# Kernel optimization log

Measured on AMD Instinct MI355X. Metric: run time of the kernel, lower is better.

Reference implementation:

```python
import jax, jax.numpy as jnp
import numpy as np

B, S, H = 1, 2048, 1024
NH, HD = 16, 64          # num heads, head dim (H = NH*HD)
NT = 1024                # param token num (qkv_slot_num = proj_slot_num)


def pattention(x, key_tokens, value_tokens):
    """Pattention with gelu_l2_norm: x:[...,H] -> [...,out]."""
    attn = jnp.einsum('bsh,th->bst', x, key_tokens)          # scale_factor = 1
    g = jax.nn.gelu(attn, approximate=False)                 # torch F.gelu exact
    norm = jnp.linalg.norm(g, axis=-1, keepdims=True)
    w = g / norm * jnp.sqrt(jnp.asarray(g.shape[-1], g.dtype))
    return jnp.einsum('bst,td->bsd', w, value_tokens)


def setup_inputs() -> dict:
    key = jax.random.key(0)
    ks = jax.random.split(key, 9)
    names = ['q_key', 'q_val', 'k_key', 'k_val', 'v_key', 'v_val', 'proj_key', 'proj_val']
    inp = {'x': jax.random.normal(ks[0], (B, S, H), jnp.float32)}
    for i, n in enumerate(names):
        inp[n] = jax.random.normal(ks[i + 1], (NT, H), jnp.float32) * 0.02
    return inp


def reference(x, q_key, q_val, k_key, k_val, v_key, v_val, proj_key, proj_val):
    # Q/K/V via Pattention (token-parameter attention)
    q = pattention(x, q_key, q_val).reshape(B, S, NH, HD)
    k = pattention(x, k_key, k_val).reshape(B, S, NH, HD)
    v = pattention(x, v_key, v_val).reshape(B, S, NH, HD)
    # causal softmax attention, scale = 1/sqrt(head_dim) (flash default)
    scale = 1.0 / jnp.sqrt(jnp.asarray(HD, q.dtype))
    scores = jnp.einsum('bqhd,bkhd->bhqk', q, k) * scale
    causal = jnp.tril(jnp.ones((S, S), dtype=bool))
    scores = jnp.where(causal, scores, jnp.asarray(-1e30, scores.dtype))
    probs = jax.nn.softmax(scores, axis=-1)
    ctx = jnp.einsum('bhqk,bkhd->bqhd', probs, v).reshape(B, S, H)
    # output projection via Pattention
    return pattention(ctx, proj_key, proj_val)
```

## Files before the change

### kernel.cpp

```cpp
#include <hip/hip_runtime.h>
#include <cstdint>
#include <cstddef>

#define S_LEN 2048
#define H_DIM 1024
#define NTOK  1024
#define NHEAD 16
#define HDIM  64

typedef __bf16 bf16;
typedef __bf16 bf16x8 __attribute__((ext_vector_type(8)));
typedef __bf16 bf16x4 __attribute__((ext_vector_type(4)));
typedef float  f32x4  __attribute__((ext_vector_type(4)));

static __device__ __forceinline__ f32x4 mfma16(bf16x8 a, bf16x8 b, f32x4 c) {
    return __builtin_amdgcn_mfma_f32_16x16x32_bf16(a, b, c, 0, 0, 0);
}

static __device__ __forceinline__ void async16(const void* gp, void* lp) {
    __builtin_amdgcn_global_load_lds(
        (const __attribute__((address_space(1))) void*)gp,
        (__attribute__((address_space(3))) void*)lp, 16, 0, 0);
}

struct ConvArgs {
    const float* src[6];
    bf16* dst[6];
};
__global__ __launch_bounds__(256) void convert6(ConvArgs a) {
    const float* __restrict__ s = a.src[blockIdx.y];
    bf16* __restrict__ d = a.dst[blockIdx.y];
    size_t i = ((size_t)blockIdx.x * 256 + threadIdx.x) * 4;
    f32x4 v = *(const f32x4*)&s[i];
    bf16x4 o;
    o[0] = (bf16)v[0]; o[1] = (bf16)v[1]; o[2] = (bf16)v[2]; o[3] = (bf16)v[3];
    *(bf16x4*)&d[i] = o;
}

struct TcArgs {
    const float* src[4];
    bf16* dst[4];
};
__global__ void transpose_cvt(TcArgs a) {
    const float* __restrict__ in = a.src[blockIdx.z];
    bf16* __restrict__ out = a.dst[blockIdx.z];
    __shared__ float t[32][33];
    const int bx = blockIdx.x * 32, by = blockIdx.y * 32;
    const int x = threadIdx.x, y = threadIdx.y;
#pragma unroll
    for (int j = 0; j < 32; j += 8)
        t[y + j][x] = in[(size_t)(by + y + j) * 1024 + bx + x];
    __syncthreads();
#pragma unroll
    for (int j = 0; j < 32; j += 8)
        out[(size_t)(bx + y + j) * 1024 + by + x] = (bf16)t[x][y + j];
}

template <int MODE, typename OutT>
struct GemmArgs {
    const bf16* A[3];
    const bf16* B[3];
    OutT* C[3];
};

template <int MODE, typename OutT>
__global__ __launch_bounds__(256, 3) void gemm_bt(GemmArgs<MODE, OutT> args) {
    constexpr int Kd = 1024, Nd = 1024, BK = 64;
    const bf16* __restrict__ A = args.A[blockIdx.z];
    const bf16* __restrict__ B = args.B[blockIdx.z];
    OutT* __restrict__ C = args.C[blockIdx.z];

    __shared__ __align__(16) bf16 As[2][128 * BK];
    __shared__ __align__(16) bf16 Bs[2][64 * BK];

    const int tid = threadIdx.x;
    const int w = tid >> 6, lane = tid & 63, quad = lane >> 4, m16 = lane & 15;
    const int wm = (w >> 1) * 64, wn = (w & 1) * 32;
    const int bm = blockIdx.y * 128, bn = blockIdx.x * 64;

    const int srow = lane >> 3;
    const int sseg = ((lane & 7) ^ srow) * 8;

    auto stage = [&](int buf, int k0) {
        const bf16* Ab = A + (size_t)bm * Kd + k0;
#pragma unroll
        for (int c = 0; c < 4; ++c) {
            int chunk = w * 4 + c;
            async16(Ab + (size_t)(chunk * 8 + srow) * Kd + sseg,
                    &As[buf][chunk * 512]);
        }
        const bf16* Bb = B + (size_t)bn * Kd + k0;
#pragma unroll
        for (int c = 0; c < 2; ++c) {
            int chunk = w * 2 + c;
            async16(Bb + (size_t)(chunk * 8 + srow) * Kd + sseg,
                    &Bs[buf][chunk * 512]);
        }
    };

    f32x4 acc[4][2] = {};
    stage(0, 0);

    for (int k0 = 0; k0 < Kd; k0 += BK) {
        const int buf = (k0 >> 6) & 1;
        asm volatile("s_waitcnt vmcnt(0)" ::: "memory");
        __syncthreads();
        if (k0 + BK < Kd) stage(buf ^ 1, k0 + BK);

        bf16x8 a[2][4], b[2][2];
#pragma unroll
        for (int kc = 0; kc < 2; ++kc) {
#pragma unroll
            for (int i = 0; i < 4; ++i) {
                int row = wm + i * 16 + m16;
                a[kc][i] = *(const bf16x8*)
                    &As[buf][row * 64 + (((kc * 4 + quad) ^ (row & 7)) << 3)];
            }
#pragma unroll
            for (int j = 0; j < 2; ++j) {
                int row = wn + j * 16 + m16;
                b[kc][j] = *(const bf16x8*)
                    &Bs[buf][row * 64 + (((kc * 4 + quad) ^ (row & 7)) << 3)];
            }
        }
#pragma unroll
        for (int kc = 0; kc < 2; ++kc)
#pragma unroll
            for (int i = 0; i < 4; ++i)
#pragma unroll
                for (int j = 0; j < 2; ++j)
                    acc[i][j] = mfma16(a[kc][i], b[kc][j], acc[i][j]);
    }

#pragma unroll
    for (int i = 0; i < 4; ++i)
#pragma unroll
        for (int j = 0; j < 2; ++j)
#pragma unroll
            for (int r = 0; r < 4; ++r) {
                int row = bm + wm + i * 16 + quad * 4 + r;
                int col = bn + wn + j * 16 + m16;
                float v = acc[i][j][r];
                if (MODE == 1)
                    v = 0.5f * v * (1.0f + erff(v * 0.70710678118654752f));
                C[(size_t)row * Nd + col] = (OutT)v;
            }
}

struct NormArgs { bf16* G[3]; };
__global__ __launch_bounds__(256) void rownorm_kernel(NormArgs na) {
    __shared__ float wsum[4];
    bf16* __restrict__ G = na.G[blockIdx.y];
    const int s = blockIdx.x, tid = threadIdx.x;
    bf16* row = G + (size_t)s * 1024;
    bf16x4 g = *(const bf16x4*)&row[tid * 4];
    float f0 = (float)g[0], f1 = (float)g[1], f2 = (float)g[2], f3 = (float)g[3];
    float ss = f0 * f0 + f1 * f1 + f2 * f2 + f3 * f3;
#pragma unroll
    for (int sh = 1; sh < 64; sh <<= 1) ss += __shfl_xor(ss, sh);
    if ((tid & 63) == 0) wsum[tid >> 6] = ss;
    __syncthreads();
    float total = wsum[0] + wsum[1] + wsum[2] + wsum[3];
    float scale = 32.0f * rsqrtf(total);
    bf16x4 o;
    o[0] = (bf16)(f0 * scale); o[1] = (bf16)(f1 * scale);
    o[2] = (bf16)(f2 * scale); o[3] = (bf16)(f3 * scale);
    *(bf16x4*)&row[tid * 4] = o;
}

__global__ __launch_bounds__(256, 3) void flash_kernel(
    const bf16* __restrict__ Q, const bf16* __restrict__ K,
    const bf16* __restrict__ V, bf16* __restrict__ Opart,
    float* __restrict__ ml) {
    const int pr = blockIdx.x, h = blockIdx.y, s = blockIdx.z;
    const int tid = threadIdx.x;
    const int w = tid >> 6, lane = tid & 63, quad = lane >> 4, m16 = lane & 15;
    const int hOff = h * HDIM;

    __shared__ __align__(16) bf16 Vt[64 * 64];
    __shared__ __align__(16) bf16 Pw[4][16][72];

    const int vd8 = (tid & 7) * 8;
    const int vkk = tid >> 3;

#pragma unroll
    for (int ti = 0; ti < 2; ++ti) {
        const int qt = ti ? 31 - pr : pr;
        const int qRow = qt * 64 + w * 16 + m16;
        bf16x8 aq[2];
        aq[0] = *(const bf16x8*)&Q[(size_t)qRow * H_DIM + hOff + quad * 8];
        aq[1] = *(const bf16x8*)&Q[(size_t)qRow * H_DIM + hOff + 32 + quad * 8];

        f32x4 oacc[4] = {};
        float m_i[4], l_i[4];
#pragma unroll
        for (int r = 0; r < 4; ++r) { m_i[r] = -1e30f; l_i[r] = 0.0f; }

        for (int kt = s; kt <= qt; kt += 3) {
            const int k0 = kt * 64;
            const bool diag = (kt == qt);
            __syncthreads();
#pragma unroll
            for (int p = 0; p < 2; ++p) {
                int kk = vkk + p * 32;
                bf16x8 v = *(const bf16x8*)&V[(size_t)(k0 + kk) * H_DIM + hOff + vd8];
#pragma unroll
                for (int e = 0; e < 8; ++e)
                    Vt[(vd8 + e) * 64 + (kk ^ vd8)] = v[e];
            }
            f32x4 sacc[4] = {};
#pragma unroll
            for (int ks = 0; ks < 2; ++ks)
#pragma unroll
                for (int j = 0; j < 4; ++j) {
                    bf16x8 bk = *(const bf16x8*)
                        &K[(size_t)(k0 + j * 16 + m16) * H_DIM + hOff + ks * 32 + quad * 8];
                    sacc[j] = mfma16(aq[ks], bk, sacc[j]);
                }
            float alpha[4];
#pragma unroll
            for (int r = 0; r < 4; ++r) {
                const int row = qt * 64 + w * 16 + quad * 4 + r;
                float sv[4], mx = -1e30f;
#pragma unroll
                for (int j = 0; j < 4; ++j) {
                    float sc = sacc[j][r] * 0.125f;
                    if (diag && (k0 + j * 16 + m16) > row) sc = -1e30f;
                    sv[j] = sc;
                    mx = fmaxf(mx, sc);
                }
#pragma unroll
                for (int sh = 1; sh < 16; sh <<= 1) mx = fmaxf(mx, __shfl_xor(mx, sh));
                float mnew = fmaxf(m_i[r], mx);
                alpha[r] = __expf(m_i[r] - mnew);
                m_i[r] = mnew;
                float ls = 0.0f;
#pragma unroll
                for (int j = 0; j < 4; ++j) {
                    float p = __expf(sv[j] - mnew);
                    ls += p;
                    Pw[w][quad * 4 + r][j * 16 + m16] = (bf16)p;
                }
#pragma unroll
                for (int sh = 1; sh < 16; sh <<= 1) ls += __shfl_xor(ls, sh);
                l_i[r] = l_i[r] * alpha[r] + ls;
#pragma unroll
                for (int jd = 0; jd < 4; ++jd) oacc[jd][r] *= alpha[r];
            }
            __syncthreads();
#pragma unroll
            for (int ks = 0; ks < 2; ++ks) {
                bf16x8 ap = *(const bf16x8*)&Pw[w][m16][ks * 32 + quad * 8];
#pragma unroll
                for (int jd = 0; jd < 4; ++jd) {
                    int d = jd * 16 + m16;
                    bf16x8 bv = *(const bf16x8*)
                        &Vt[d * 64 + ((ks * 32 + quad * 8) ^ (d & 56))];
                    oacc[jd] = mfma16(ap, bv, oacc[jd]);
                }
            }
        }
#pragma unroll
        for (int r = 0; r < 4; ++r) {
            const int row = qt * 64 + w * 16 + quad * 4 + r;
#pragma unroll
            for (int jd = 0; jd < 4; ++jd)
                Opart[(size_t)(s * 2048 + row) * 1024 + hOff + jd * 16 + m16] =
                    (bf16)oacc[jd][r];
            if (m16 == 0) {
                float* p = ml + ((size_t)(s * 2048 + row) * 16 + h) * 2;
                p[0] = m_i[r];
                p[1] = l_i[r];
            }
        }
    }
}

__global__ __launch_bounds__(256) void combine_kernel(
    const bf16* __restrict__ Opart, const float* __restrict__ ml,
    bf16* __restrict__ ctx) {
    const int unit = blockIdx.x * 4 + (threadIdx.x >> 6);
    const int row = unit >> 4, h = unit & 15;
    const int d = threadIdx.x & 63;
    float mv[3], lv[3], M = -1e30f;
#pragma unroll
    for (int s2 = 0; s2 < 3; ++s2) {
        const float* p = ml + ((size_t)(s2 * 2048 + row) * 16 + h) * 2;
        mv[s2] = p[0];
        lv[s2] = p[1];
        M = fmaxf(M, mv[s2]);
    }
    float num = 0.0f, den = 0.0f;
#pragma unroll
    for (int s2 = 0; s2 < 3; ++s2) {
        float e = __expf(mv[s2] - M);
        den += lv[s2] * e;
        num += e * (float)Opart[(size_t)(s2 * 2048 + row) * 1024 + h * 64 + d];
    }
    ctx[(size_t)row * 1024 + h * 64 + d] = (bf16)(num / den);
}

extern "C" void kernel_launch(void* const* d_in, const int* in_sizes, int n_in,
                              void* d_out, int out_size, void* d_ws,
                              size_t ws_size, hipStream_t stream) {
    const float* x = (const float*)d_in[0];
    const float* keysF[4] = {(const float*)d_in[1], (const float*)d_in[3],
                             (const float*)d_in[5], (const float*)d_in[7]};
    const float* valsF[4] = {(const float*)d_in[2], (const float*)d_in[4],
                             (const float*)d_in[6], (const float*)d_in[8]};
    float* out = (float*)d_out;

    char* ws = (char*)d_ws;
    bf16* xb = (bf16*)(ws);
    bf16* g3[3];
    for (int i = 0; i < 3; ++i) g3[i] = (bf16*)(ws + (4ull << 20) + (size_t)i * (4ull << 20));
    bf16* kb16[4], *vT16[4];
    for (int i = 0; i < 4; ++i) {
        kb16[i] = (bf16*)(ws + (16ull << 20) + (size_t)i * (2ull << 20));
        vT16[i] = (bf16*)(ws + (24ull << 20) + (size_t)i * (2ull << 20));
    }
    bf16* qb    = (bf16*)(ws);
    bf16* kbuf  = (bf16*)(ws + (32ull << 20));
    bf16* vbuf  = (bf16*)(ws + (36ull << 20));
    bf16* Opart = (bf16*)(ws + (4ull << 20));
    bf16* ctx   = (bf16*)(ws + (32ull << 20));
    bf16* projg = (bf16*)(ws + (4ull << 20));
    float* mlbuf = (float*)d_out;

    ConvArgs ca;
    ca.src[0] = x;             ca.dst[0] = xb;
    ca.src[1] = x + (1 << 20); ca.dst[1] = xb + (1 << 20);
    for (int i = 0; i < 4; ++i) { ca.src[2 + i] = keysF[i]; ca.dst[2 + i] = kb16[i]; }
    convert6<<<dim3(1024, 6), 256, 0, stream>>>(ca);

    TcArgs ta;
    for (int i = 0; i < 4; ++i) { ta.src[i] = valsF[i]; ta.dst[i] = vT16[i]; }
    transpose_cvt<<<dim3(32, 32, 4), dim3(32, 8), 0, stream>>>(ta);

    GemmArgs<1, bf16> g1;
    for (int z = 0; z < 3; ++z) { g1.A[z] = xb; g1.B[z] = kb16[z]; g1.C[z] = g3[z]; }
    gemm_bt<1, bf16><<<dim3(16, 16, 3), 256, 0, stream>>>(g1);

    NormArgs na;
    for (int z = 0; z < 3; ++z) na.G[z] = g3[z];
    rownorm_kernel<<<dim3(2048, 3), 256, 0, stream>>>(na);

    GemmArgs<0, bf16> g2;
    bf16* qkv[3] = {qb, kbuf, vbuf};
    for (int z = 0; z < 3; ++z) { g2.A[z] = g3[z]; g2.B[z] = vT16[z]; g2.C[z] = qkv[z]; }
    gemm_bt<0, bf16><<<dim3(16, 16, 3), 256, 0, stream>>>(g2);

    flash_kernel<<<dim3(16, 16, 3), 256, 0, stream>>>(qb, kbuf, vbuf, Opart, mlbuf);

    combine_kernel<<<dim3(8192), 256, 0, stream>>>(Opart, mlbuf, ctx);

    GemmArgs<1, bf16> p1;
    p1.A[0] = ctx; p1.B[0] = kb16[3]; p1.C[0] = projg;
    for (int z = 1; z < 3; ++z) { p1.A[z] = ctx; p1.B[z] = kb16[3]; p1.C[z] = projg; }
    gemm_bt<1, bf16><<<dim3(16, 16, 1), 256, 0, stream>>>(p1);

    NormArgs np;
    for (int z = 0; z < 3; ++z) np.G[z] = projg;
    rownorm_kernel<<<dim3(2048, 1), 256, 0, stream>>>(np);

    GemmArgs<0, float> p2;
    for (int z = 0; z < 3; ++z) { p2.A[z] = projg; p2.B[z] = vT16[3]; p2.C[z] = out; }
    gemm_bt<0, float><<<dim3(16, 16, 1), 256, 0, stream>>>(p2);
}
```

Baseline: 246.7 us.

## Pre-transpose V globally and raise flash KV split count to four

A new kernel writes V transposed per head into global memory. The flash kernel can then load V operands for the PV MFMA straight into registers, with no per-tile LDS staging and one fewer block barrier per KV tile. The KV split grows from 3 to 4 and the launch-bounds occupancy hint rises to 4, for more parallelism. The cost is an extra launch, an extra V read/write pass, and a larger partial-output buffer for the combine step.

```diff
diff --git a/kernel.cpp b/kernel.cpp
--- a/kernel.cpp
+++ b/kernel.cpp
@@ -7,6 +7,7 @@
 #define NTOK  1024
 #define NHEAD 16
 #define HDIM  64
+#define NSPLIT 4
 
 typedef __bf16 bf16;
 typedef __bf16 bf16x8 __attribute__((ext_vector_type(8)));
@@ -56,6 +57,30 @@
         out[(size_t)(bx + y + j) * 1024 + by + x] = (bf16)t[x][y + j];
 }
 
+__global__ __launch_bounds__(256) void vtrans_kernel(const bf16* __restrict__ V,
+                                                     bf16* __restrict__ Vt) {
+    const int k0 = blockIdx.x * 64, h = blockIdx.y;
+    const int tid = threadIdx.x;
+    __shared__ __align__(16) bf16 tile[64 * 64];
+    const int kk = tid >> 3, d8 = (tid & 7) * 8;
+#pragma unroll
+    for (int p = 0; p < 2; ++p) {
+        int k = kk + p * 32;
+        bf16x8 v = *(const bf16x8*)&V[(size_t)(k0 + k) * H_DIM + h * 64 + d8];
+#pragma unroll
+        for (int e = 0; e < 8; ++e)
+            tile[(d8 + e) * 64 + (k ^ ((d8 + e) & 56))] = v[e];
+    }
+    __syncthreads();
+    const int d = tid >> 2;
+#pragma unroll
+    for (int c = 0; c < 2; ++c) {
+        int k8 = ((tid & 3) * 2 + c) * 8;
+        bf16x8 v = *(const bf16x8*)&tile[d * 64 + (k8 ^ (d & 56))];
+        *(bf16x8*)&Vt[((size_t)(h * 64 + d)) * 2048 + k0 + k8] = v;
+    }
+}
+
 template <int MODE, typename OutT>
 struct GemmArgs {
     const bf16* A[3];
@@ -168,20 +193,16 @@
     *(bf16x4*)&row[tid * 4] = o;
 }
 
-__global__ __launch_bounds__(256, 3) void flash_kernel(
+__global__ __launch_bounds__(256, 4) void flash_kernel(
     const bf16* __restrict__ Q, const bf16* __restrict__ K,
-    const bf16* __restrict__ V, bf16* __restrict__ Opart,
+    const bf16* __restrict__ Vt, bf16* __restrict__ Opart,
     float* __restrict__ ml) {
     const int pr = blockIdx.x, h = blockIdx.y, s = blockIdx.z;
     const int tid = threadIdx.x;
     const int w = tid >> 6, lane = tid & 63, quad = lane >> 4, m16 = lane & 15;
     const int hOff = h * HDIM;
 
-    __shared__ __align__(16) bf16 Vt[64 * 64];
     __shared__ __align__(16) bf16 Pw[4][16][72];
-
-    const int vd8 = (tid & 7) * 8;
-    const int vkk = tid >> 3;
 
 #pragma unroll
     for (int ti = 0; ti < 2; ++ti) {
@@ -196,18 +217,9 @@
 #pragma unroll
         for (int r = 0; r < 4; ++r) { m_i[r] = -1e30f; l_i[r] = 0.0f; }
 
-        for (int kt = s; kt <= qt; kt += 3) {
+        for (int kt = s; kt <= qt; kt += NSPLIT) {
             const int k0 = kt * 64;
             const bool diag = (kt == qt);
-            __syncthreads();
-#pragma unroll
-            for (int p = 0; p < 2; ++p) {
-                int kk = vkk + p * 32;
-                bf16x8 v = *(const bf16x8*)&V[(size_t)(k0 + kk) * H_DIM + hOff + vd8];
-#pragma unroll
-                for (int e = 0; e < 8; ++e)
-                    Vt[(vd8 + e) * 64 + (kk ^ vd8)] = v[e];
-            }
             f32x4 sacc[4] = {};
 #pragma unroll
             for (int ks = 0; ks < 2; ++ks)
@@ -217,6 +229,13 @@
                         &K[(size_t)(k0 + j * 16 + m16) * H_DIM + hOff + ks * 32 + quad * 8];
                     sacc[j] = mfma16(aq[ks], bk, sacc[j]);
                 }
+            bf16x8 bv[2][4];
+#pragma unroll
+            for (int ks = 0; ks < 2; ++ks)
+#pragma unroll
+                for (int jd = 0; jd < 4; ++jd)
+                    bv[ks][jd] = *(const bf16x8*)
+                        &Vt[(size_t)(hOff + jd * 16 + m16) * 2048 + k0 + ks * 32 + quad * 8];
             float alpha[4];
 #pragma unroll
             for (int r = 0; r < 4; ++r) {
@@ -247,17 +266,13 @@
 #pragma unroll
                 for (int jd = 0; jd < 4; ++jd) oacc[jd][r] *= alpha[r];
             }
-            __syncthreads();
+            asm volatile("s_waitcnt lgkmcnt(0)" ::: "memory");
 #pragma unroll
             for (int ks = 0; ks < 2; ++ks) {
                 bf16x8 ap = *(const bf16x8*)&Pw[w][m16][ks * 32 + quad * 8];
 #pragma unroll
-                for (int jd = 0; jd < 4; ++jd) {
-                    int d = jd * 16 + m16;
-                    bf16x8 bv = *(const bf16x8*)
-                        &Vt[d * 64 + ((ks * 32 + quad * 8) ^ (d & 56))];
-                    oacc[jd] = mfma16(ap, bv, oacc[jd]);
-                }
+                for (int jd = 0; jd < 4; ++jd)
+                    oacc[jd] = mfma16(ap, bv[ks][jd], oacc[jd]);
             }
         }
 #pragma unroll
@@ -282,9 +297,9 @@
     const int unit = blockIdx.x * 4 + (threadIdx.x >> 6);
     const int row = unit >> 4, h = unit & 15;
     const int d = threadIdx.x & 63;
-    float mv[3], lv[3], M = -1e30f;
-#pragma unroll
-    for (int s2 = 0; s2 < 3; ++s2) {
+    float mv[NSPLIT], lv[NSPLIT], M = -1e30f;
+#pragma unroll
+    for (int s2 = 0; s2 < NSPLIT; ++s2) {
         const float* p = ml + ((size_t)(s2 * 2048 + row) * 16 + h) * 2;
         mv[s2] = p[0];
         lv[s2] = p[1];
@@ -292,7 +307,7 @@
     }
     float num = 0.0f, den = 0.0f;
 #pragma unroll
-    for (int s2 = 0; s2 < 3; ++s2) {
+    for (int s2 = 0; s2 < NSPLIT; ++s2) {
         float e = __expf(mv[s2] - M);
         den += lv[s2] * e;
         num += e * (float)Opart[(size_t)(s2 * 2048 + row) * 1024 + h * 64 + d];
@@ -323,6 +338,7 @@
     bf16* kbuf  = (bf16*)(ws + (32ull << 20));
     bf16* vbuf  = (bf16*)(ws + (36ull << 20));
     bf16* Opart = (bf16*)(ws + (4ull << 20));
+    bf16* VtG   = (bf16*)(ws + (24ull << 20));
     bf16* ctx   = (bf16*)(ws + (32ull << 20));
     bf16* projg = (bf16*)(ws + (4ull << 20));
     float* mlbuf = (float*)d_out;
@@ -350,13 +366,14 @@
     for (int z = 0; z < 3; ++z) { g2.A[z] = g3[z]; g2.B[z] = vT16[z]; g2.C[z] = qkv[z]; }
     gemm_bt<0, bf16><<<dim3(16, 16, 3), 256, 0, stream>>>(g2);
 
-    flash_kernel<<<dim3(16, 16, 3), 256, 0, stream>>>(qb, kbuf, vbuf, Opart, mlbuf);
+    vtrans_kernel<<<dim3(32, 16), 256, 0, stream>>>(vbuf, VtG);
+
+    flash_kernel<<<dim3(16, 16, NSPLIT), 256, 0, stream>>>(qb, kbuf, VtG, Opart, mlbuf);
 
     combine_kernel<<<dim3(8192), 256, 0, stream>>>(Opart, mlbuf, ctx);
 
     GemmArgs<1, bf16> p1;
-    p1.A[0] = ctx; p1.B[0] = kb16[3]; p1.C[0] = projg;
-    for (int z = 1; z < 3; ++z) { p1.A[z] = ctx; p1.B[z] = kb16[3]; p1.C[z] = projg; }
+    for (int z = 0; z < 3; ++z) { p1.A[z] = ctx; p1.B[z] = kb16[3]; p1.C[z] = projg; }
     gemm_bt<1, bf16><<<dim3(16, 16, 1), 256, 0, stream>>>(p1);
 
     NormArgs np;
```

Result: slower. 267.9 us (+8.6%).
